# Optimization experiments

Measured on AMD Instinct MI355X. Metric: run time of the kernel, lower is better.

The kernel has to match this reference:

```python
import jax, jax.numpy as jnp
import numpy as np
import math

E = 256      # embed_dim
H = 16       # num_heads
D = E // H   # qkv_dim
MSH = 16     # ms_hidden_dim
B, R, C = 2, 512, 512


def setup_inputs() -> dict:
    key = jax.random.key(0)
    ks = jax.random.split(key, 10)
    x1 = jax.random.normal(ks[0], (B, R, E), jnp.float32)
    x2 = jax.random.normal(ks[1], (B, C, E), jnp.float32)
    attn_mask = jax.random.randint(ks[2], (B, R, C), 0, 2) > 0  # True = valid
    cost_mat = jax.random.uniform(ks[3], (B, R, C), jnp.float32)
    # torch nn.Linear default init ~ U(-1/sqrt(fan_in), 1/sqrt(fan_in))
    def lin(k, out_d, in_d, bound):
        return jax.random.uniform(k, (out_d, in_d), jnp.float32, -bound, bound)
    Wqv1 = lin(ks[4], 2 * E, E, 1.0 / math.sqrt(E))
    Wkv2 = lin(ks[5], 2 * E, E, 1.0 / math.sqrt(E))
    W1 = lin(ks[6], H * MSH, 2 * H, math.sqrt(0.5))       # mix1_init
    W2 = lin(ks[7], H, H * MSH, math.sqrt(1.0 / MSH))      # mix2_init
    Wout1 = lin(ks[8], E, E, 1.0 / math.sqrt(E))
    Wout2 = lin(ks[9], E, E, 1.0 / math.sqrt(E))
    return {"x1": x1, "x2": x2, "attn_mask": attn_mask, "cost_mat": cost_mat,
            "Wqv1": Wqv1, "Wkv2": Wkv2, "W1": W1, "W2": W2,
            "Wout1": Wout1, "Wout2": Wout2}


def _apply_weights_and_combine(logits, v, mask):
    # mask: True = masked out; rows fully masked are un-masked (torch clone trick)
    all_masked = jnp.all(mask, axis=-1, keepdims=True)
    mask = jnp.where(all_masked, False, mask)
    logits = jnp.where(mask, -jnp.inf, logits)
    w = jax.nn.softmax(logits, axis=-1)          # [b,h,r,c]
    out = jnp.einsum('bhrc,bhcd->bhrd', w, v)     # [b,h,r,d]
    b, h, r, d = out.shape
    return out.transpose(0, 2, 1, 3).reshape(b, r, h * d)  # b s (h d)


def reference(x1, x2, attn_mask, cost_mat, Wqv1, Wkv2, W1, W2, Wout1, Wout2):
    b, r, _ = x1.shape
    c = x2.shape[1]
    # q, v1 from x1 ; k, v2 from x2
    qv = (x1 @ Wqv1.T).reshape(b, r, 2, H, D)
    q = qv[:, :, 0].transpose(0, 2, 1, 3)   # [b,h,r,d]
    v1 = qv[:, :, 1].transpose(0, 2, 1, 3)
    kv = (x2 @ Wkv2.T).reshape(b, c, 2, H, D)
    k = kv[:, :, 0].transpose(0, 2, 1, 3)   # [b,h,c,d]
    v2 = kv[:, :, 1].transpose(0, 2, 1, 3)

    dot = jnp.einsum('bhrd,bhcd->bhrc', q, k) * (1.0 / math.sqrt(D))
    cost = jnp.broadcast_to(cost_mat[:, None], dot.shape)  # [b,h,r,c]

    # MixedScoreFF: stack -> [b,h,r,c,2] -> [b,r,c,2h] -> MLP -> [b,r,c,h]
    two = jnp.stack((dot, cost), axis=-1)
    two = two.transpose(0, 2, 3, 1, 4).reshape(b, r, c, 2 * H)
    ms = jax.nn.relu(two @ W1.T) @ W2.T      # [b,r,c,H]
    ms1 = ms.transpose(0, 3, 1, 2)            # [b,h,r,c]
    ms2 = ms1.transpose(0, 1, 3, 2)           # [b,h,c,r]

    mask1 = jnp.broadcast_to(~attn_mask[:, None], (b, H, r, c))  # True = masked
    mask2 = mask1.transpose(0, 1, 3, 2)

    h1 = _apply_weights_and_combine(ms1, v2, mask1) @ Wout1.T  # [b,r,E]
    h2 = _apply_weights_and_combine(ms2, v1, mask2) @ Wout2.T  # [b,c,E]
    return (h1, h2)
```

## Files before the change

### kernel.cpp

```cpp
#include <hip/hip_runtime.h>
#include <hip/hip_bf16.h>

typedef unsigned int   u32;
typedef unsigned short u16;

typedef __attribute__((ext_vector_type(8))) short    sh8;
typedef __attribute__((ext_vector_type(4))) float    f32x4;
typedef __attribute__((ext_vector_type(8))) _Float16 f16x8;
typedef __attribute__((ext_vector_type(2))) _Float16 f16x2;
typedef __attribute__((ext_vector_type(2))) __fp16   fp16x2raw;

union F16x8 { f16x8 v; uint4 u; f16x2 p[4]; _Float16 h[8]; };
union F16x4u { uint2 u; _Float16 h[4]; };
union F16x2u { u32 u; _Float16 h[2]; };
union CvtU  { fp16x2raw r; f16x2 p; u32 u; };

__device__ __forceinline__ float b2f(u16 u) { union { u32 i; float f; } v; v.i = ((u32)u) << 16; return v.f; }
__device__ __forceinline__ u16   f2b(float f){
  union { float f; u32 i; } v; v.f = f;
  u32 u = v.i;
  u32 r = (u + 0x7fffu + ((u >> 16) & 1u)) >> 16;
  return (u16)r;
}
__device__ __forceinline__ u32 pk2(float a, float b) {
  __hip_bfloat162 h2 = __float22bfloat162_rn(make_float2(a, b));
  union { __hip_bfloat162 h; u32 u; } v; v.h = h2; return v.u;
}
__device__ __forceinline__ f16x2 cvtpk(float a, float b) {
  CvtU c; c.r = __builtin_amdgcn_cvt_pkrtz(a, b); return c.p;
}
__device__ __forceinline__ u32 cvtpku(float a, float b) {
  CvtU c; c.r = __builtin_amdgcn_cvt_pkrtz(a, b); return c.u;
}

__device__ __forceinline__ f32x4 mfma16(uint4 a, uint4 b, f32x4 c) {
  union { uint4 u; sh8 s; } ua, ub;
  ua.u = a; ub.u = b;
  return __builtin_amdgcn_mfma_f32_16x16x32_bf16(ua.s, ub.s, c, 0, 0, 0);
}
__device__ __forceinline__ f32x4 mfma32h(f16x8 a, f16x8 b, f32x4 c) {
  return __builtin_amdgcn_mfma_f32_16x16x32_f16(a, b, c, 0, 0, 0);
}

__device__ __forceinline__ void split8(float4 v0, float4 v1, uint4& hi, uint4& lo) {
  float a[8] = {v0.x, v0.y, v0.z, v0.w, v1.x, v1.y, v1.z, v1.w};
  u32 hw[4], lw[4];
#pragma unroll
  for (int t = 0; t < 4; t++) {
    u32 hp = pk2(a[2 * t], a[2 * t + 1]);
    float r0 = a[2 * t]     - __uint_as_float(hp << 16);
    float r1 = a[2 * t + 1] - __uint_as_float(hp & 0xffff0000u);
    hw[t] = hp;
    lw[t] = pk2(r0, r1);
  }
  hi = make_uint4(hw[0], hw[1], hw[2], hw[3]);
  lo = make_uint4(lw[0], lw[1], lw[2], lw[3]);
}

__global__ void __launch_bounds__(256)
gemm_mf(const float* __restrict__ A0, const float* __restrict__ B0, float* __restrict__ C0,
        const float* __restrict__ A1, const float* __restrict__ B1, float* __restrict__ C1,
        int N, int K) {
  __shared__ __align__(16) uint4 BH[32 * 17];
  __shared__ __align__(16) uint4 BL[32 * 17];
  int t = threadIdx.x, L = t & 63, w = t >> 6;
  int cl = L & 15, q = L >> 4;
  int by = blockIdx.y, sel = by >> 4;
  const float* A  = sel ? A1 : A0;
  const float* Bw = sel ? B1 : B0;
  float*       C  = sel ? C1 : C0;
  int m0 = (by & 15) * 64 + w * 16;
  int n0 = blockIdx.x * 16;

  for (int e = t; e < 512; e += 256) {
    int chunk = e >> 4, row = e & 15;
    const float* bp = Bw + (size_t)(n0 + row) * K + chunk * 8;
    float4 b0 = *(const float4*)bp;
    float4 b1 = *(const float4*)(bp + 4);
    uint4 hi, lo;
    split8(b0, b1, hi, lo);
    BH[chunk * 17 + row] = hi;
    BL[chunk * 17 + row] = lo;
  }
  __syncthreads();

  f32x4 acc; acc[0] = 0.f; acc[1] = 0.f; acc[2] = 0.f; acc[3] = 0.f;
  const float* ar = A + (size_t)(m0 + cl) * K + 8 * q;

  for (int k0 = 0; k0 < K; k0 += 32) {
    float4 av0 = *(const float4*)(ar + k0);
    float4 av1 = *(const float4*)(ar + k0 + 4);
    uint4 ahi, alo;
    split8(av0, av1, ahi, alo);
    uint4 bhi = BH[((k0 >> 3) + q) * 17 + cl];
    uint4 blo = BL[((k0 >> 3) + q) * 17 + cl];
    acc = mfma16(ahi, bhi, acc);
    acc = mfma16(ahi, blo, acc);
    acc = mfma16(alo, bhi, acc);
  }
#pragma unroll
  for (int i = 0; i < 4; i++)
    C[(size_t)(m0 + 4 * q + i) * N + n0 + cl] = acc[i];
}

__global__ void __launch_bounds__(256)
gemm_mf_pack(const float* __restrict__ x1, const float* __restrict__ Wqv1, u16* __restrict__ vhT1,
             const float* __restrict__ x2, const float* __restrict__ Wkv2, u16* __restrict__ vhT2,
             const float* __restrict__ W1, const float* __restrict__ W2,
             uint4* __restrict__ QQ4, uint4* __restrict__ KH4, uint4* __restrict__ KL4z,
             uint4* __restrict__ W1F8hi, uint4* __restrict__ W1F8lo,
             uint4* __restrict__ W2F8hi, uint4* __restrict__ W2F8lo) {
  __shared__ float Ld[4][16][17];
  __shared__ __align__(16) uint4 BH[32 * 17];
  __shared__ __align__(16) uint4 BL[32 * 17];
  int t = threadIdx.x, L = t & 63, w = t >> 6;
  int cl = L & 15, q = L >> 4;
  int by = blockIdx.y;

  if (by == 32) {
    if (blockIdx.x >= 8) return;
    int tid = blockIdx.x * 256 + t;
    if (tid < 1024) {
      int LL = tid & 63, nt = tid >> 6;
      int j = nt * 16 + (LL & 15), qq = LL >> 4;
      F16x8 hi, lo;
#pragma unroll
      for (int jj = 0; jj < 8; jj++) {
        float wv = W1[j * 32 + qq * 8 + jj];
        hi.h[jj] = (_Float16)wv;
        lo.h[jj] = (_Float16)(wv - (float)hi.h[jj]);
      }
      W1F8hi[tid] = hi.u;
      W1F8lo[tid] = lo.u;
    } else if (tid < 1536) {
      int t2 = tid - 1024;
      int LL = t2 & 63, p = t2 >> 6;
      int h = LL & 15, qq = LL >> 4;
      F16x8 hi, lo;
#pragma unroll
      for (int jj = 0; jj < 8; jj++) {
        int j = 32 * p + ((jj >> 2) << 4) + 4 * qq + (jj & 3);
        float wv = W2[h * 256 + j];
        hi.h[jj] = (_Float16)wv;
        lo.h[jj] = (_Float16)(wv - (float)hi.h[jj]);
      }
      W2F8hi[t2] = hi.u;
      W2F8lo[t2] = lo.u;
    }
    return;
  }

  int sel = by >> 4;
  const float* A  = sel ? x2 : x1;
  const float* Bw = sel ? Wkv2 : Wqv1;
  int m0 = (by & 15) * 64 + w * 16;
  int n0 = blockIdx.x * 16;

  for (int e = t; e < 512; e += 256) {
    int chunk = e >> 4, row = e & 15;
    const float* bp = Bw + (size_t)(n0 + row) * 256 + chunk * 8;
    float4 b0 = *(const float4*)bp;
    float4 b1 = *(const float4*)(bp + 4);
    uint4 hi, lo;
    split8(b0, b1, hi, lo);
    BH[chunk * 17 + row] = hi;
    BL[chunk * 17 + row] = lo;
  }
  __syncthreads();

  f32x4 acc; acc[0] = 0.f; acc[1] = 0.f; acc[2] = 0.f; acc[3] = 0.f;
  const float* ar = A + (size_t)(m0 + cl) * 256 + 8 * q;

  for (int k0 = 0; k0 < 256; k0 += 32) {
    float4 av0 = *(const float4*)(ar + k0);
    float4 av1 = *(const float4*)(ar + k0 + 4);
    uint4 ahi, alo;
    split8(av0, av1, ahi, alo);
    uint4 bhi = BH[((k0 >> 3) + q) * 17 + cl];
    uint4 blo = BL[((k0 >> 3) + q) * 17 + cl];
    acc = mfma16(ahi, bhi, acc);
    acc = mfma16(ahi, blo, acc);
    acc = mfma16(alo, bhi, acc);
  }

  int b = m0 >> 9;
  int row = (m0 & 511) + cl;

  if (n0 >= 256) {
#pragma unroll
    for (int i = 0; i < 4; i++) Ld[w][cl][4 * q + i] = acc[i];
    if (q < 2) {
      float vt[8];
#pragma unroll
      for (int jj = 0; jj < 8; jj++) vt[jj] = Ld[w][cl][q * 8 + jj];
      uint4 o = make_uint4(cvtpku(vt[0], vt[1]), cvtpku(vt[2], vt[3]),
                           cvtpku(vt[4], vt[5]), cvtpku(vt[6], vt[7]));
      u16* vT = sel ? vhT2 : vhT1;
      *(uint4*)(vT + ((size_t)(b * 256) + (n0 - 256) + cl) * 512 + (m0 & 511) + 8 * q) = o;
    }
    return;
  }

#pragma unroll
  for (int i = 0; i < 4; i++) Ld[w][cl][4 * q + i] = acc[i];
  float v[8];
#pragma unroll
  for (int jj = 0; jj < 8; jj++) v[jj] = Ld[w][(q & 1) * 8 + jj][cl];

  int r = row;
  int h = n0 >> 4;

  if (sel == 0) {
    u32 wv[4];
#pragma unroll
    for (int t2 = 0; t2 < 4; t2++) {
      float a  = v[2 * t2] * 0.25f, bb = v[2 * t2 + 1] * 0.25f;
      u32 hp = pk2(a, bb);
      if (q >= 2) {
        float r0 = a  - __uint_as_float(hp << 16);
        float r1 = bb - __uint_as_float(hp & 0xffff0000u);
        wv[t2] = pk2(r0, r1);
      } else wv[t2] = hp;
    }
    QQ4[((size_t)((b * 16 + h) * 4 + q) << 9) + r] = make_uint4(wv[0], wv[1], wv[2], wv[3]);
  } else {
    u32 hw[4], lw[4];
#pragma unroll
    for (int t2 = 0; t2 < 4; t2++) {
      float a = v[2 * t2], bb = v[2 * t2 + 1];
      u32 hp = pk2(a, bb);
      float r0 = a  - __uint_as_float(hp << 16);
      float r1 = bb - __uint_as_float(hp & 0xffff0000u);
      hw[t2] = hp;
      lw[t2] = pk2(r0, r1);
    }
    if (q < 2) {
      KH4[((size_t)((b * 16 + h) * 2 + q) << 9) + r]       = make_uint4(hw[0], hw[1], hw[2], hw[3]);
      KL4z[((size_t)((b * 16 + h) * 4 + 2 + q) << 9) + r]  = make_uint4(0, 0, 0, 0);
    } else {
      KL4z[((size_t)((b * 16 + h) * 4 + (q - 2)) << 9) + r] = make_uint4(lw[0], lw[1], lw[2], lw[3]);
    }
  }
}

__global__ void __launch_bounds__(256, 4)
ms_mfma8c(const uint4* __restrict__ QQ4, const uint4* __restrict__ KH4,
          const uint4* __restrict__ KL4z, const float* __restrict__ cost,
          const uint4* __restrict__ W1F8hi, const uint4* __restrict__ W1F8lo,
          const uint4* __restrict__ W2F8hi, const uint4* __restrict__ W2F8lo,
          u16* __restrict__ ms1, u16* __restrict__ ms2) {
  __shared__ __align__(16) u32 Dl[2 * 2176];
  int t = threadIdx.x, L = t & 63, w = t >> 6;
  int cl = L & 15, q = L >> 4;
  int b = blockIdx.z, c0 = blockIdx.y * 16;
  int pairId = w >> 1, wl = w & 1;
  int r0a = blockIdx.x * 32 + pairId * 16;
  int r0  = r0a + wl * 8;
  u32* D = Dl + pairId * 2176;

  f32x4 z; z[0] = 0.f; z[1] = 0.f; z[2] = 0.f; z[3] = 0.f;

  float cvh[8];
#pragma unroll
  for (int rr = 0; rr < 8; rr++)
    cvh[rr] = cost[((size_t)(b * 512) + r0 + rr) * 512 + c0 + cl];

#pragma unroll 2
  for (int hpi = 0; hpi < 4; hpi++) {
    int hp = wl * 4 + hpi;
    int h0 = 2 * hp, h1 = 2 * hp + 1;
    uint4 qa  = QQ4[((size_t)((b * 16 + h0) * 4 + q) << 9) + r0a + cl];
    uint4 qa2 = QQ4[((size_t)((b * 16 + h0) * 4 + (q & 1)) << 9) + r0a + cl];
    uint4 kb1 = KH4[((size_t)((b * 16 + h0) * 2 + (q & 1)) << 9) + c0 + cl];
    uint4 kb2 = KL4z[((size_t)((b * 16 + h0) * 4 + q) << 9) + c0 + cl];
    f32x4 d0 = mfma16(qa, kb1, z);
    d0 = mfma16(qa2, kb2, d0);
    uint4 qb  = QQ4[((size_t)((b * 16 + h1) * 4 + q) << 9) + r0a + cl];
    uint4 qb2 = QQ4[((size_t)((b * 16 + h1) * 4 + (q & 1)) << 9) + r0a + cl];
    uint4 kc1 = KH4[((size_t)((b * 16 + h1) * 2 + (q & 1)) << 9) + c0 + cl];
    uint4 kc2 = KL4z[((size_t)((b * 16 + h1) * 4 + q) << 9) + c0 + cl];
    f32x4 d1 = mfma16(qb, kc1, z);
    d1 = mfma16(qb2, kc2, d1);
#pragma unroll
    for (int i = 0; i < 4; i++)
      D[(4 * q + i) * 136 + hp * 17 + cl] = cvtpku(d0[i], d1[i]);
  }
  __syncthreads();

  F16x8 xv[8];
#pragma unroll
  for (int rr = 0; rr < 8; rr++) {
    int rl = wl * 8 + rr;
    u32 ch = cvtpku(0.f, cvh[rr]);
    u32 ua = D[rl * 136 + (2 * q) * 17 + cl];
    u32 ub = D[rl * 136 + (2 * q + 1) * 17 + cl];
    xv[rr].u = make_uint4((ua & 0xffffu) | ch, (ua >> 16) | ch,
                          (ub & 0xffffu) | ch, (ub >> 16) | ch);
  }

  f32x4 acc2[8];
#pragma unroll
  for (int rr = 0; rr < 8; rr++) acc2[rr] = z;

  F16x8 w1h0, w1h1, w2h, w2l;
  w1h0.u = W1F8hi[0 * 64 + L];
  w1h1.u = W1F8hi[1 * 64 + L];
  w2h.u  = W2F8hi[0 * 64 + L];
  w2l.u  = W2F8lo[0 * 64 + L];

#pragma unroll 1
  for (int p = 0; p < 8; p++) {
    int pn = (p + 1) & 7;
    F16x8 nw0, nw1, n2h, n2l;
    nw0.u = W1F8hi[(2 * pn) * 64 + L];
    nw1.u = W1F8hi[(2 * pn + 1) * 64 + L];
    n2h.u = W2F8hi[pn * 64 + L];
    n2l.u = W2F8lo[pn * 64 + L];
#pragma unroll
    for (int rr = 0; rr < 8; rr++) {
      f32x4 a0 = mfma32h(w1h0.v, xv[rr].v, z);
      f32x4 a1 = mfma32h(w1h1.v, xv[rr].v, z);
      F16x8 hf;
      hf.p[0] = cvtpk(fmaxf(a0[0], 0.f), fmaxf(a0[1], 0.f));
      hf.p[1] = cvtpk(fmaxf(a0[2], 0.f), fmaxf(a0[3], 0.f));
      hf.p[2] = cvtpk(fmaxf(a1[0], 0.f), fmaxf(a1[1], 0.f));
      hf.p[3] = cvtpk(fmaxf(a1[2], 0.f), fmaxf(a1[3], 0.f));
      acc2[rr] = mfma32h(hf.v, w2h.v, acc2[rr]);
      acc2[rr] = mfma32h(hf.v, w2l.v, acc2[rr]);
    }
    w1h0 = nw0; w1h1 = nw1; w2h = n2h; w2l = n2l;
  }

  u32* ms1u = (u32*)ms1;
#pragma unroll
  for (int rr = 0; rr < 8; rr++) {
    size_t base = ((size_t)(b * 16 + cl) * 512 + (r0 + rr)) * 256 + (c0 >> 1) + q * 2;
    ms1u[base]     = pk2(acc2[rr][0], acc2[rr][1]);
    ms1u[base + 1] = pk2(acc2[rr][2], acc2[rr][3]);
  }
  u32* ms2u = (u32*)ms2;
#pragma unroll
  for (int i = 0; i < 4; i++) {
    int c = c0 + 4 * q + i;
    u32 o[4];
#pragma unroll
    for (int j = 0; j < 4; j++)
      o[j] = pk2(acc2[2 * j][i], acc2[2 * j + 1][i]);
    size_t base2 = ((size_t)(b * 16 + cl) * 512 + c) * 256 + (r0 >> 1);
    *(uint4*)&ms2u[base2] = make_uint4(o[0], o[1], o[2], o[3]);
  }
}

__global__ void __launch_bounds__(256, 4)
softmax_pv_mf(const u16* __restrict__ ms1s, const u16* __restrict__ ms2s,
              const int* __restrict__ mask,
              const u16* __restrict__ vhT1, const u16* __restrict__ vhT2,
              float* __restrict__ o1, float* __restrict__ o2) {
  __shared__ __align__(16) char pbufc[4][8192];
  __shared__ unsigned char maskbytes[8][64];
  __shared__ float sden[4][8];
  int t = threadIdx.x, L = t & 63, w = t >> 6;
  int cl = L & 15, q = L >> 4;
  int bx = blockIdx.x;
  int u  = (bx & 7) + 8 * ((bx >> 3) & 1);
  int v  = (bx >> 4) & 3;
  int hq = bx >> 6;
  int rt = u * 4 + v;
  int b = blockIdx.y, dir = blockIdx.z;
  int fix0 = rt * 8, h = hq * 4 + w;
  const u16* ms = dir ? ms2s : ms1s;

  if (dir == 0) {
#pragma unroll
    for (int fo = 0; fo < 2; fo++) {
      int f = 2 * w + fo;
      const int* mr = mask + ((size_t)(b * 512) + fix0 + f) * 512 + 8 * L;
      uint4 m0 = *(const uint4*)mr;
      uint4 m1 = *(const uint4*)(mr + 4);
      u32 bits = (u32)(m0.x != 0)        | ((u32)(m0.y != 0) << 1)
               | ((u32)(m0.z != 0) << 2) | ((u32)(m0.w != 0) << 3)
               | ((u32)(m1.x != 0) << 4) | ((u32)(m1.y != 0) << 5)
               | ((u32)(m1.z != 0) << 6) | ((u32)(m1.w != 0) << 7);
      maskbytes[f][L] = (unsigned char)bits;
    }
  } else {
    u32 b0 = 0, b1 = 0;
#pragma unroll
    for (int j = 0; j < 8; j++) {
      const int* mp = mask + ((size_t)(b * 512) + 8 * L + j) * 512 + fix0 + 2 * w;
      uint2 mv = *(const uint2*)mp;
      b0 |= (u32)(mv.x != 0) << j;
      b1 |= (u32)(mv.y != 0) << j;
    }
    maskbytes[2 * w][L]     = (unsigned char)b0;
    maskbytes[2 * w + 1][L] = (unsigned char)b1;
  }
  __syncthreads();

  const u16* msbase = ms + ((size_t)((b * 16 + h) * 512) + fix0) * 512 + 8 * L;
  uint4 pre[8];
#pragma unroll
  for (int f = 0; f < 8; f++) pre[f] = *(const uint4*)(msbase + f * 512);

  char* pb = pbufc[w];
#pragma unroll
  for (int f = 0; f < 8; f++) {
    u32 uw[4] = {pre[f].x, pre[f].y, pre[f].z, pre[f].w};
    float lg[8];
#pragma unroll
    for (int j = 0; j < 4; j++) {
      lg[2 * j]     = __uint_as_float(uw[j] << 16);
      lg[2 * j + 1] = __uint_as_float(uw[j] & 0xffff0000u);
    }
    u32 mb = (u32)maskbytes[f][L];
    bool um = (__ballot(mb != 0) != 0ULL);
    u32 eff = um ? mb : 0xffu;
    float mx = -3.4e38f;
#pragma unroll
    for (int j = 0; j < 8; j++)
      mx = fmaxf(mx, ((eff >> j) & 1) ? lg[j] : -3.4e38f);
    for (int off = 32; off; off >>= 1) mx = fmaxf(mx, __shfl_xor(mx, off));
    float s = 0.f; u32 pw[4];
#pragma unroll
    for (int j = 0; j < 4; j++) {
      float p0 = ((eff >> (2 * j)) & 1)     ? __expf(lg[2 * j]     - mx) : 0.f;
      float p1 = ((eff >> (2 * j + 1)) & 1) ? __expf(lg[2 * j + 1] - mx) : 0.f;
      s += p0 + p1;
      pw[j] = cvtpku(p0, p1);
    }
    for (int off = 32; off; off >>= 1) s += __shfl_xor(s, off);
    if (L == 0) sden[w][f] = s;
    *(uint4*)(pb + f * 1024 + ((16 * L) ^ (f << 4))) = make_uint4(pw[0], pw[1], pw[2], pw[3]);
  }

  const u16* vT = (dir ? vhT1 : vhT2) + ((size_t)(b * 256 + h * 16 + cl) * 512) + 8 * q;
  f32x4 accA; accA[0] = 0.f; accA[1] = 0.f; accA[2] = 0.f; accA[3] = 0.f;
  f32x4 accB = accA;
  int ar = (cl & 7);
#pragma unroll
  for (int kk = 0; kk < 16; kk++) {
    F16x8 pa, vb;
    pa.u = *(const uint4*)(pb + ar * 1024 + (((kk << 6) + (q << 4)) ^ (ar << 4)));
    vb.u = *(const uint4*)(vT + (kk << 5));
    if (kk & 1) accB = mfma32h(pa.v, vb.v, accB);
    else        accA = mfma32h(pa.v, vb.v, accA);
  }

  if (q < 2) {
    float* obuf = dir ? o2 : o1;
#pragma unroll
    for (int i = 0; i < 4; i++) {
      int f = 4 * q + i;
      float inv = 1.f / sden[w][f];
      obuf[((size_t)(b * 512) + fix0 + f) * 256 + h * 16 + cl] = (accA[i] + accB[i]) * inv;
    }
  }
}

extern "C" void kernel_launch(void* const* d_in, const int* in_sizes, int n_in,
                              void* d_out, int out_size, void* d_ws, size_t ws_size,
                              hipStream_t stream) {
  const float* x1    = (const float*)d_in[0];
  const float* x2    = (const float*)d_in[1];
  const int*   attn  = (const int*)d_in[2];
  const float* cost  = (const float*)d_in[3];
  const float* Wqv1  = (const float*)d_in[4];
  const float* Wkv2  = (const float*)d_in[5];
  const float* W1    = (const float*)d_in[6];
  const float* W2    = (const float*)d_in[7];
  const float* Wout1 = (const float*)d_in[8];
  const float* Wout2 = (const float*)d_in[9];
  float* out = (float*)d_out;

  char* ws = (char*)d_ws;
  uint4* W1F8hi = (uint4*)(ws);
  uint4* W1F8lo = (uint4*)(ws + (16 << 10));
  uint4* W2F8hi = (uint4*)(ws + (32 << 10));
  uint4* W2F8lo = (uint4*)(ws + (40 << 10));
  u16*   vhT1 = (u16*)(ws + (64 << 10));
  u16*   vhT2 = (u16*)(ws + (64 << 10) + (512 << 10));
  u16*   ms1 = (u16*)(ws + (64 << 10) + (4 << 20));
  u16*   ms2 = (u16*)(ws + (64 << 10) + (20 << 20));
  char*  tail= (ws + (64 << 10) + (36 << 20));
  uint4* QQ4  = (uint4*)(tail);
  uint4* KH4  = (uint4*)(tail + (1 << 20));
  uint4* KL4z = (uint4*)(tail + (1 << 20) + (512 << 10));
  float* o1  = (float*)(tail + (3 << 20));
  float* o2  = (float*)(tail + (4 << 20));

  gemm_mf_pack<<<dim3(32, 33), 256, 0, stream>>>(x1, Wqv1, vhT1, x2, Wkv2, vhT2,
                                                 W1, W2, QQ4, KH4, KL4z,
                                                 W1F8hi, W1F8lo, W2F8hi, W2F8lo);

  ms_mfma8c<<<dim3(16, 32, 2), 256, 0, stream>>>(QQ4, KH4, KL4z, cost,
                                                 W1F8hi, W1F8lo, W2F8hi, W2F8lo, ms1, ms2);

  softmax_pv_mf<<<dim3(256, 2, 2), 256, 0, stream>>>(ms1, ms2, attn, vhT1, vhT2, o1, o2);

  gemm_mf<<<dim3(16, 32), 256, 0, stream>>>(o1, Wout1, out, o2, Wout2, out + (size_t)262144, 256, 256);
}
```

Measured before the change: 134.9 us.

## Widen projection GEMM tiles to 32 columns and stage A in LDS for output GEMM

The QKV projection kernel now computes two 16-column output tiles per wave, so each A row is loaded and split into hi/lo bf16 once per 32 columns instead of once per 16, and the grid is halved. The output projection GEMM is replaced by a 32x32 tiled kernel that stages both A and B, split into hi/lo, in padded LDS, cutting redundant global loads and splits of A. The cost is more LDS per block and more registers per thread, which may lower occupancy; both kernels are a small part of the total pipeline.

```diff
diff --git a/kernel.cpp b/kernel.cpp
--- a/kernel.cpp
+++ b/kernel.cpp
@@ -58,49 +58,56 @@
 }
 
 __global__ void __launch_bounds__(256)
-gemm_mf(const float* __restrict__ A0, const float* __restrict__ B0, float* __restrict__ C0,
-        const float* __restrict__ A1, const float* __restrict__ B1, float* __restrict__ C1,
-        int N, int K) {
-  __shared__ __align__(16) uint4 BH[32 * 17];
-  __shared__ __align__(16) uint4 BL[32 * 17];
+gemm_mf2t(const float* __restrict__ o1, const float* __restrict__ o2,
+          const float* __restrict__ Wout1, const float* __restrict__ Wout2,
+          float* __restrict__ out) {
+  __shared__ __align__(16) uint4 AH[32 * 33];
+  __shared__ __align__(16) uint4 AL[32 * 33];
+  __shared__ __align__(16) uint4 BH[32 * 33];
+  __shared__ __align__(16) uint4 BL[32 * 33];
   int t = threadIdx.x, L = t & 63, w = t >> 6;
   int cl = L & 15, q = L >> 4;
-  int by = blockIdx.y, sel = by >> 4;
-  const float* A  = sel ? A1 : A0;
-  const float* Bw = sel ? B1 : B0;
-  float*       C  = sel ? C1 : C0;
-  int m0 = (by & 15) * 64 + w * 16;
-  int n0 = blockIdx.x * 16;
-
-  for (int e = t; e < 512; e += 256) {
-    int chunk = e >> 4, row = e & 15;
-    const float* bp = Bw + (size_t)(n0 + row) * K + chunk * 8;
+  int by = blockIdx.y, sel = by >> 5, mb = by & 31;
+  int m0 = mb * 32, n0 = blockIdx.x * 32;
+  const float* A  = sel ? o2 : o1;
+  const float* Bw = sel ? Wout2 : Wout1;
+
+  for (int e = t; e < 1024; e += 256) {
+    int chunk = e & 31, row = e >> 5;
+    const float* ap = A + (size_t)(m0 + row) * 256 + chunk * 8;
+    float4 a0 = *(const float4*)ap;
+    float4 a1 = *(const float4*)(ap + 4);
+    uint4 hi, lo;
+    split8(a0, a1, hi, lo);
+    AH[chunk * 33 + row] = hi;
+    AL[chunk * 33 + row] = lo;
+    const float* bp = Bw + (size_t)(n0 + row) * 256 + chunk * 8;
     float4 b0 = *(const float4*)bp;
     float4 b1 = *(const float4*)(bp + 4);
-    uint4 hi, lo;
     split8(b0, b1, hi, lo);
-    BH[chunk * 17 + row] = hi;
-    BL[chunk * 17 + row] = lo;
+    BH[chunk * 33 + row] = hi;
+    BL[chunk * 33 + row] = lo;
   }
   __syncthreads();
 
+  int wm = w >> 1, wn = w & 1;
+  int ma = 16 * wm + cl, na = 16 * wn + cl;
   f32x4 acc; acc[0] = 0.f; acc[1] = 0.f; acc[2] = 0.f; acc[3] = 0.f;
-  const float* ar = A + (size_t)(m0 + cl) * K + 8 * q;
-
-  for (int k0 = 0; k0 < K; k0 += 32) {
-    float4 av0 = *(const float4*)(ar + k0);
-    float4 av1 = *(const float4*)(ar + k0 + 4);
-    uint4 ahi, alo;
-    split8(av0, av1, ahi, alo);
-    uint4 bhi = BH[((k0 >> 3) + q) * 17 + cl];
-    uint4 blo = BL[((k0 >> 3) + q) * 17 + cl];
+#pragma unroll
+  for (int k0 = 0; k0 < 256; k0 += 32) {
+    int cb = ((k0 >> 3) + q) * 33;
+    uint4 ahi = AH[cb + ma];
+    uint4 alo = AL[cb + ma];
+    uint4 bhi = BH[cb + na];
+    uint4 blo = BL[cb + na];
     acc = mfma16(ahi, bhi, acc);
     acc = mfma16(ahi, blo, acc);
     acc = mfma16(alo, bhi, acc);
   }
+  float* C = out + (size_t)sel * 262144;
 #pragma unroll
   for (int i = 0; i < 4; i++)
-    C[(size_t)(m0 + 4 * q + i) * N + n0 + cl] = acc[i];
+    C[(size_t)(m0 + 16 * wm + 4 * q + i) * 256 + n0 + 16 * wn + cl] = acc[i];
 }
 
 __global__ void __launch_bounds__(256)
@@ -111,8 +118,8 @@
              uint4* __restrict__ W1F8hi, uint4* __restrict__ W1F8lo,
              uint4* __restrict__ W2F8hi, uint4* __restrict__ W2F8lo) {
   __shared__ float Ld[4][16][17];
-  __shared__ __align__(16) uint4 BH[32 * 17];
-  __shared__ __align__(16) uint4 BL[32 * 17];
+  __shared__ __align__(16) uint4 BH[32 * 33];
+  __shared__ __align__(16) uint4 BL[32 * 33];
   int t = threadIdx.x, L = t & 63, w = t >> 6;
   int cl = L & 15, q = L >> 4;
   int by = blockIdx.y;
@@ -154,21 +161,22 @@
   const float* A  = sel ? x2 : x1;
   const float* Bw = sel ? Wkv2 : Wqv1;
   int m0 = (by & 15) * 64 + w * 16;
-  int n0 = blockIdx.x * 16;
-
-  for (int e = t; e < 512; e += 256) {
-    int chunk = e >> 4, row = e & 15;
+  int n0 = blockIdx.x * 32;
+
+  for (int e = t; e < 1024; e += 256) {
+    int chunk = e & 31, row = e >> 5;
     const float* bp = Bw + (size_t)(n0 + row) * 256 + chunk * 8;
     float4 b0 = *(const float4*)bp;
     float4 b1 = *(const float4*)(bp + 4);
     uint4 hi, lo;
     split8(b0, b1, hi, lo);
-    BH[chunk * 17 + row] = hi;
-    BL[chunk * 17 + row] = lo;
+    BH[chunk * 33 + row] = hi;
+    BL[chunk * 33 + row] = lo;
   }
   __syncthreads();
 
-  f32x4 acc; acc[0] = 0.f; acc[1] = 0.f; acc[2] = 0.f; acc[3] = 0.f;
+  f32x4 acc0; acc0[0] = 0.f; acc0[1] = 0.f; acc0[2] = 0.f; acc0[3] = 0.f;
+  f32x4 acc1 = acc0;
   const float* ar = A + (size_t)(m0 + cl) * 256 + 8 * q;
 
   for (int k0 = 0; k0 < 256; k0 += 32) {
@@ -176,69 +184,79 @@
     float4 av1 = *(const float4*)(ar + k0 + 4);
     uint4 ahi, alo;
     split8(av0, av1, ahi, alo);
-    uint4 bhi = BH[((k0 >> 3) + q) * 17 + cl];
-    uint4 blo = BL[((k0 >> 3) + q) * 17 + cl];
-    acc = mfma16(ahi, bhi, acc);
-    acc = mfma16(ahi, blo, acc);
-    acc = mfma16(alo, bhi, acc);
+    int cb = ((k0 >> 3) + q) * 33;
+    uint4 bhi0 = BH[cb + cl],      blo0 = BL[cb + cl];
+    uint4 bhi1 = BH[cb + 16 + cl], blo1 = BL[cb + 16 + cl];
+    acc0 = mfma16(ahi, bhi0, acc0);
+    acc0 = mfma16(ahi, blo0, acc0);
+    acc0 = mfma16(alo, bhi0, acc0);
+    acc1 = mfma16(ahi, bhi1, acc1);
+    acc1 = mfma16(ahi, blo1, acc1);
+    acc1 = mfma16(alo, bhi1, acc1);
   }
 
   int b = m0 >> 9;
   int row = (m0 & 511) + cl;
 
-  if (n0 >= 256) {
+#pragma unroll
+  for (int ti = 0; ti < 2; ti++) {
+    f32x4 acc = ti ? acc1 : acc0;
+    int n0p = n0 + 16 * ti;
+
+    if (n0p >= 256) {
+#pragma unroll
+      for (int i = 0; i < 4; i++) Ld[w][cl][4 * q + i] = acc[i];
+      if (q < 2) {
+        float vt[8];
+#pragma unroll
+        for (int jj = 0; jj < 8; jj++) vt[jj] = Ld[w][cl][q * 8 + jj];
+        uint4 o = make_uint4(cvtpku(vt[0], vt[1]), cvtpku(vt[2], vt[3]),
+                             cvtpku(vt[4], vt[5]), cvtpku(vt[6], vt[7]));
+        u16* vT = sel ? vhT2 : vhT1;
+        *(uint4*)(vT + ((size_t)(b * 256) + (n0p - 256) + cl) * 512 + (m0 & 511) + 8 * q) = o;
+      }
+      continue;
+    }
+
 #pragma unroll
     for (int i = 0; i < 4; i++) Ld[w][cl][4 * q + i] = acc[i];
-    if (q < 2) {
-      float vt[8];
-#pragma unroll
-      for (int jj = 0; jj < 8; jj++) vt[jj] = Ld[w][cl][q * 8 + jj];
-      uint4 o = make_uint4(cvtpku(vt[0], vt[1]), cvtpku(vt[2], vt[3]),
-                           cvtpku(vt[4], vt[5]), cvtpku(vt[6], vt[7]));
-      u16* vT = sel ? vhT2 : vhT1;
-      *(uint4*)(vT + ((size_t)(b * 256) + (n0 - 256) + cl) * 512 + (m0 & 511) + 8 * q) = o;
-    }
-    return;
-  }
-
-#pragma unroll
-  for (int i = 0; i < 4; i++) Ld[w][cl][4 * q + i] = acc[i];
-  float v[8];
-#pragma unroll
-  for (int jj = 0; jj < 8; jj++) v[jj] = Ld[w][(q & 1) * 8 + jj][cl];
-
-  int r = row;
-  int h = n0 >> 4;
-
-  if (sel == 0) {
-    u32 wv[4];
-#pragma unroll
-    for (int t2 = 0; t2 < 4; t2++) {
-      float a  = v[2 * t2] * 0.25f, bb = v[2 * t2 + 1] * 0.25f;
-      u32 hp = pk2(a, bb);
-      if (q >= 2) {
+    float v[8];
+#pragma unroll
+    for (int jj = 0; jj < 8; jj++) v[jj] = Ld[w][(q & 1) * 8 + jj][cl];
+
+    int r = row;
+    int h = n0p >> 4;
+
+    if (sel == 0) {
+      u32 wv[4];
+#pragma unroll
+      for (int t2 = 0; t2 < 4; t2++) {
+        float a  = v[2 * t2] * 0.25f, bb = v[2 * t2 + 1] * 0.25f;
+        u32 hp = pk2(a, bb);
+        if (q >= 2) {
+          float r0 = a  - __uint_as_float(hp << 16);
+          float r1 = bb - __uint_as_float(hp & 0xffff0000u);
+          wv[t2] = pk2(r0, r1);
+        } else wv[t2] = hp;
+      }
+      QQ4[((size_t)((b * 16 + h) * 4 + q) << 9) + r] = make_uint4(wv[0], wv[1], wv[2], wv[3]);
+    } else {
+      u32 hw[4], lw[4];
+#pragma unroll
+      for (int t2 = 0; t2 < 4; t2++) {
+        float a = v[2 * t2], bb = v[2 * t2 + 1];
+        u32 hp = pk2(a, bb);
         float r0 = a  - __uint_as_float(hp << 16);
         float r1 = bb - __uint_as_float(hp & 0xffff0000u);
-        wv[t2] = pk2(r0, r1);
-      } else wv[t2] = hp;
-    }
-    QQ4[((size_t)((b * 16 + h) * 4 + q) << 9) + r] = make_uint4(wv[0], wv[1], wv[2], wv[3]);
-  } else {
-    u32 hw[4], lw[4];
-#pragma unroll
-    for (int t2 = 0; t2 < 4; t2++) {
-      float a = v[2 * t2], bb = v[2 * t2 + 1];
-      u32 hp = pk2(a, bb);
-      float r0 = a  - __uint_as_float(hp << 16);
-      float r1 = bb - __uint_as_float(hp & 0xffff0000u);
-      hw[t2] = hp;
-      lw[t2] = pk2(r0, r1);
-    }
-    if (q < 2) {
-      KH4[((size_t)((b * 16 + h) * 2 + q) << 9) + r]       = make_uint4(hw[0], hw[1], hw[2], hw[3]);
-      KL4z[((size_t)((b * 16 + h) * 4 + 2 + q) << 9) + r]  = make_uint4(0, 0, 0, 0);
-    } else {
-      KL4z[((size_t)((b * 16 + h) * 4 + (q - 2)) << 9) + r] = make_uint4(lw[0], lw[1], lw[2], lw[3]);
+        hw[t2] = hp;
+        lw[t2] = pk2(r0, r1);
+      }
+      if (q < 2) {
+        KH4[((size_t)((b * 16 + h) * 2 + q) << 9) + r]       = make_uint4(hw[0], hw[1], hw[2], hw[3]);
+        KL4z[((size_t)((b * 16 + h) * 4 + 2 + q) << 9) + r]  = make_uint4(0, 0, 0, 0);
+      } else {
+        KL4z[((size_t)((b * 16 + h) * 4 + (q - 2)) << 9) + r] = make_uint4(lw[0], lw[1], lw[2], lw[3]);
+      }
     }
   }
 }
@@ -488,7 +506,7 @@
   float* o1  = (float*)(tail + (3 << 20));
   float* o2  = (float*)(tail + (4 << 20));
 
-  gemm_mf_pack<<<dim3(32, 33), 256, 0, stream>>>(x1, Wqv1, vhT1, x2, Wkv2, vhT2,
+  gemm_mf_pack<<<dim3(16, 33), 256, 0, stream>>>(x1, Wqv1, vhT1, x2, Wkv2, vhT2,
                                                  W1, W2, QQ4, KH4, KL4z,
                                                  W1F8hi, W1F8lo, W2F8hi, W2F8lo);
 
@@ -497,5 +515,5 @@
 
   softmax_pv_mf<<<dim3(256, 2, 2), 256, 0, stream>>>(ms1, ms2, attn, vhT1, vhT2, o1, o2);
 
-  gemm_mf<<<dim3(16, 32), 256, 0, stream>>>(o1, Wout1, out, o2, Wout2, out + (size_t)262144, 256, 256);
-}
+  gemm_mf2t<<<dim3(8, 64), 256, 0, stream>>>(o1, o2, Wout1, Wout2, out);
+}
```

New measurement: 130.9 us. 3.0% less time.
